# Performance work log

Measured on AMD Instinct MI355X. Metric: run time of the kernel, lower is better.

The kernel has to match this reference:

```python
import jax, jax.numpy as jnp
import numpy as np

WS = 7
NUM_HEADS = 12
DIM = 384
HEAD_DIM = DIM // NUM_HEADS
SCALE = HEAD_DIM ** -0.5


def _rel_pos_index(ws: int) -> jnp.ndarray:
    coords = np.stack(np.meshgrid(np.arange(ws), np.arange(ws), indexing='ij'))  # (2, ws, ws)
    cf = coords.reshape(2, -1)                       # (2, ws*ws)
    rel = cf[:, :, None] - cf[:, None, :]            # (2, N, N)
    rel = rel.transpose(1, 2, 0).copy()              # (N, N, 2)
    rel[..., 0] += ws - 1
    rel[..., 1] += ws - 1
    rel[..., 0] *= 2 * ws - 1
    return jnp.asarray(rel.sum(-1))                  # (N, N) int indices into bias table


REL_IDX = _rel_pos_index(WS)


def setup_inputs() -> dict:
    key = jax.random.key(0)
    ks = jax.random.split(key, 7)
    BW, N, C = 4096, WS * WS, DIM
    num_win = 64
    return {
        'x': jax.random.normal(ks[0], (BW, N, C), jnp.float32),
        'mask': jax.random.normal(ks[1], (num_win, N, N), jnp.float32),
        'qkv_w': jax.random.normal(ks[2], (3 * C, C), jnp.float32) * 0.02,
        'qkv_b': jax.random.normal(ks[3], (3 * C,), jnp.float32) * 0.02,
        'proj_w': jax.random.normal(ks[4], (C, C), jnp.float32) * 0.02,
        'proj_b': jax.random.normal(ks[5], (C,), jnp.float32) * 0.02,
        'bias_table': jax.random.normal(ks[6], ((2 * WS - 1) ** 2, NUM_HEADS), jnp.float32) * 0.02,
    }


def reference(x, mask, qkv_w, qkv_b, proj_w, proj_b, bias_table):
    BW, N, C = x.shape
    H, hd = NUM_HEADS, HEAD_DIM
    # QKV projection: (BW, N, 3C) -> (3, BW, H, N, hd)
    qkv = (x @ qkv_w.T + qkv_b).reshape(BW, N, 3, H, hd).transpose(2, 0, 3, 1, 4)
    q, k, v = qkv[0], qkv[1], qkv[2]
    attn = jnp.einsum('bhnd,bhmd->bhnm', q, k) * SCALE  # (BW, H, N, N)
    bias = bias_table[REL_IDX]                          # (N, N, H)
    attn = attn + bias.transpose(2, 0, 1)[None]
    num_win = mask.shape[0]
    attn = attn.reshape(BW // num_win, num_win, H, N, N) + mask[None, :, None]
    attn = attn.reshape(BW, H, N, N)
    attn = jax.nn.softmax(attn, axis=-1)
    out = jnp.einsum('bhnm,bhmd->bhnd', attn, v)        # (BW, H, N, hd)
    out = out.transpose(0, 2, 1, 3).reshape(BW, N, C)
    return out @ proj_w.T + proj_b
```

## Files before the change

### kernel.cpp

```cpp
#include <hip/hip_runtime.h>

typedef unsigned short u16;
typedef unsigned int u32;
typedef __attribute__((ext_vector_type(8))) short short8;
typedef __attribute__((ext_vector_type(4))) float floatx4;
typedef __attribute__((ext_vector_type(4))) unsigned int u32x4;

#define SCALE_Q 0.17677669529663687f

__device__ __forceinline__ u16 f2bf(float f) {
  u32 u = __float_as_uint(f);
  u = (u + 0x7fffu + ((u >> 16) & 1u)) >> 16;
  return (u16)u;
}

__device__ __forceinline__ void gload_lds16(const void* g, void* l) {
  __builtin_amdgcn_global_load_lds(
      (const __attribute__((address_space(1))) u32*)g,
      (__attribute__((address_space(3))) u32*)l, 16, 0, 0);
}

__device__ __forceinline__ floatx4 mfma16(short8 a, short8 b, floatx4 c) {
  return __builtin_amdgcn_mfma_f32_16x16x32_bf16(a, b, c, 0, 0, 0);
}

__global__ void cast_w_kernel(const float* __restrict__ qkv_w,
                              const float* __restrict__ proj_w,
                              u16* __restrict__ wb1, u16* __restrict__ wb2) {
  int idx = blockIdx.x * 256 + threadIdx.x;
  wb1[idx] = f2bf(qkv_w[idx]);
  if (idx < 147456) wb2[idx] = f2bf(proj_w[idx]);
}

__global__ __launch_bounds__(256) void cast_x_kernel(const float* __restrict__ x,
                                                     u16* __restrict__ xb) {
  const size_t i = ((size_t)blockIdx.x * 256 + threadIdx.x) * 8;
  const float4 f0 = *(const float4*)(x + i);
  const float4 f1 = *(const float4*)(x + i + 4);
  uint4 pk;
  pk.x = (u32)f2bf(f0.x) | ((u32)f2bf(f0.y) << 16);
  pk.y = (u32)f2bf(f0.z) | ((u32)f2bf(f0.w) << 16);
  pk.z = (u32)f2bf(f1.x) | ((u32)f2bf(f1.y) << 16);
  pk.w = (u32)f2bf(f1.z) | ((u32)f2bf(f1.w) << 16);
  *(uint4*)(xb + i) = pk;
}

__global__ void comb_kernel(const float* __restrict__ bias_table,
                            const float* __restrict__ mask,
                            float* __restrict__ comb) {
  int wh = blockIdx.x;
  int w = wh / 12, h = wh - w * 12;
  float* dst = comb + (size_t)wh * 4096;
  for (int e = threadIdx.x; e < 4096; e += 256) {
    int p = e >> 6, q = e & 63;
    float v;
    if (q >= 49) v = -1e30f;
    else if (p >= 49) v = 0.0f;
    else {
      int pi = p / 7, pj = p - pi * 7;
      int qi = q / 7, qj = q - qi * 7;
      int ridx = (pi - qi + 6) * 13 + (pj - qj + 6);
      v = bias_table[ridx * 12 + h] + mask[(size_t)w * 2401 + p * 49 + q];
    }
    dst[e] = v;
  }
}

__global__ __launch_bounds__(256) void qkv_gemm(const u16* __restrict__ A,
                                                const u16* __restrict__ B,
                                                const float* __restrict__ bias,
                                                u16* __restrict__ C) {
  __shared__ u16 As[2][4096];
  __shared__ u16 Bs[2][4096];
  const int tid = threadIdx.x;
  const int lane = tid & 63;
  const int wave = tid >> 6;
  const int l15 = lane & 15;
  const int quad = lane >> 4;
  const int wr = wave >> 1, wc = wave & 1;
  const u32 bid = blockIdx.x;
  const u32 xcd = bid & 7;
  const u32 slot = bid >> 3;
  const u32 grp = slot / 9;
  const u32 tn = slot - grp * 9;
  const u32 tm = xcd * 196 + grp;

  const int c0 = tid, c1 = tid + 256;
  const int m0 = c0 >> 2, kp0 = (c0 & 3) ^ ((m0 >> 1) & 3);
  const int m1 = c1 >> 2, kp1 = (c1 & 3) ^ ((m1 >> 1) & 3);
  const u16* Ab0 = A + (size_t)(tm * 128 + m0) * 384 + kp0 * 8;
  const u16* Ab1 = A + (size_t)(tm * 128 + m1) * 384 + kp1 * 8;
  const u16* Bb0 = B + (size_t)(tn * 128 + m0) * 384 + kp0 * 8;
  const u16* Bb1 = B + (size_t)(tn * 128 + m1) * 384 + kp1 * 8;
  const int ld0 = c0 * 8, ld1 = c1 * 8;

  floatx4 acc[4][4];
#pragma unroll
  for (int i = 0; i < 4; ++i)
#pragma unroll
    for (int j = 0; j < 4; ++j) acc[i][j] = (floatx4){0.f, 0.f, 0.f, 0.f};

#define QSTAGE(buf, k0)                       \
  do {                                        \
    gload_lds16(Ab0 + (k0), &As[buf][ld0]);   \
    gload_lds16(Ab1 + (k0), &As[buf][ld1]);   \
    gload_lds16(Bb0 + (k0), &Bs[buf][ld0]);   \
    gload_lds16(Bb1 + (k0), &Bs[buf][ld1]);   \
  } while (0)

  QSTAGE(0, 0);
  __syncthreads();

  const int xq = quad ^ ((l15 >> 1) & 3);
  const int abase = (wr * 64 + l15) * 32 + xq * 8;
  const int bbase = (wc * 64 + l15) * 32 + xq * 8;
  for (int kb = 0; kb < 12; ++kb) {
    const int cur = kb & 1;
    if (kb < 11) QSTAGE(cur ^ 1, (kb + 1) * 32);
    short8 af[4], bfr[4];
#pragma unroll
    for (int i = 0; i < 4; ++i)
      af[i] = *(const short8*)(&As[cur][abase + i * 512]);
#pragma unroll
    for (int i = 0; i < 4; ++i)
      bfr[i] = *(const short8*)(&Bs[cur][bbase + i * 512]);
#pragma unroll
    for (int mi = 0; mi < 4; ++mi)
#pragma unroll
      for (int ni = 0; ni < 4; ++ni)
        acc[mi][ni] = mfma16(af[mi], bfr[ni], acc[mi][ni]);
    if (kb < 11) __syncthreads();
  }
#undef QSTAGE

#pragma unroll
  for (int ni = 0; ni < 4; ++ni) {
    const int gbase = (int)tn * 128 + wc * 64 + ni * 16;
    const int which = gbase / 384;
    const int rem = gbase - which * 384;
    const int h = rem >> 5;
    const int db = rem & 31;
    const float bb = bias[gbase + l15];
    const float scale = (which == 0) ? SCALE_Q : 1.0f;
    u16* hp = C + ((size_t)which * 49152 + h) * 1568 + db + l15;
#pragma unroll
    for (int mi = 0; mi < 4; ++mi) {
      const int grow0 = (int)tm * 128 + wr * 64 + mi * 16 + quad * 4;
#pragma unroll
      for (int r = 0; r < 4; ++r) {
        const int grow = grow0 + r;
        const int b = grow / 49;
        const int tok = grow - b * 49;
        hp[(size_t)b * 18816 + tok * 32] = f2bf((acc[mi][ni][r] + bb) * scale);
      }
    }
  }
}

__global__ __launch_bounds__(256, 2) void attn_proj(const u16* __restrict__ qkv,
                                                    const float* __restrict__ comb,
                                                    const u16* __restrict__ pw,
                                                    const float* __restrict__ pb,
                                                    float* __restrict__ out) {
  __shared__ uint4 smem[4288];
  u16* aoS = (u16*)smem;
  const int tid = threadIdx.x;
  const int lane = tid & 63;
  const int wv = tid >> 6;
  const int l15 = lane & 15, quad = lane >> 4;
  u16* Vt = (u16*)((char*)smem + 50176 + wv * 4608);

  const int bid = blockIdx.x;
  const int w = bid >> 6;
  const int b = (bid & 63) * 64 + w;

  {
    uint4* v4 = (uint4*)Vt;
    const uint4 zz = make_uint4(0u, 0u, 0u, 0u);
    for (int i = lane; i < 288; i += 64) v4[i] = zz;
  }

  const floatx4 z4 = (floatx4){0.f, 0.f, 0.f, 0.f};
  const short8 z8 = {0, 0, 0, 0, 0, 0, 0, 0};

  for (int hi = 0; hi < 3; ++hi) {
    const int h = wv + hi * 4;
    const size_t hoff = (size_t)(b * 12 + h) * 1568;
    const u16* qb = qkv + hoff;
    const u16* kbp = qkv + (size_t)49152 * 1568 + hoff;
    const u16* vb = qkv + (size_t)98304 * 1568 + hoff;

    short8 aq[4], bk[4];
#pragma unroll
    for (int i = 0; i < 3; ++i) {
      aq[i] = *(const short8*)(qb + (i * 16 + l15) * 32 + quad * 8);
      bk[i] = *(const short8*)(kbp + (i * 16 + l15) * 32 + quad * 8);
    }
    aq[3] = (l15 == 0) ? *(const short8*)(qb + 48 * 32 + quad * 8) : z8;
    bk[3] = (l15 == 0) ? *(const short8*)(kbp + 48 * 32 + quad * 8) : z8;

    for (int s0 = lane; s0 < 196; s0 += 64) {
      const int t = s0 >> 2, part = s0 & 3;
      const uint4 dv = *(const uint4*)(vb + t * 32 + part * 8);
      const int d0 = part * 8;
      const u32 vv[4] = {dv.x, dv.y, dv.z, dv.w};
#pragma unroll
      for (int e = 0; e < 4; ++e) {
        Vt[(d0 + 2 * e) * 72 + t] = (u16)(vv[e] & 0xffffu);
        Vt[(d0 + 2 * e + 1) * 72 + t] = (u16)(vv[e] >> 16);
      }
    }

    floatx4 st[4][4];
    __builtin_amdgcn_s_setprio(1);
#pragma unroll
    for (int mi = 0; mi < 4; ++mi)
#pragma unroll
      for (int ni = 0; ni < 4; ++ni) st[mi][ni] = mfma16(bk[mi], aq[ni], z4);
    __builtin_amdgcn_s_setprio(0);

    const float* cb = comb + (size_t)(w * 12 + h) * 4096;
#pragma unroll
    for (int ni = 0; ni < 4; ++ni)
#pragma unroll
      for (int mi = 0; mi < 4; ++mi) {
        const float4 cv = *(const float4*)(cb + (ni * 16 + l15) * 64 + mi * 16 + quad * 4);
        st[mi][ni][0] += cv.x;
        st[mi][ni][1] += cv.y;
        st[mi][ni][2] += cv.z;
        st[mi][ni][3] += cv.w;
      }

    float rinv[4];
#pragma unroll
    for (int ni = 0; ni < 4; ++ni) {
      float mx = st[0][ni][0];
#pragma unroll
      for (int mi = 0; mi < 4; ++mi)
#pragma unroll
        for (int r = 0; r < 4; ++r) mx = fmaxf(mx, st[mi][ni][r]);
      mx = fmaxf(mx, __shfl_xor(mx, 16));
      mx = fmaxf(mx, __shfl_xor(mx, 32));
      float sum = 0.f;
#pragma unroll
      for (int mi = 0; mi < 4; ++mi)
#pragma unroll
        for (int r = 0; r < 4; ++r) {
          const float e = __expf(st[mi][ni][r] - mx);
          st[mi][ni][r] = e;
          sum += e;
        }
      sum += __shfl_xor(sum, 16);
      sum += __shfl_xor(sum, 32);
      rinv[ni] = 1.0f / sum;
    }

    u32 pk[4][4][2];
#pragma unroll
    for (int mi = 0; mi < 4; ++mi)
#pragma unroll
      for (int ni = 0; ni < 4; ++ni)
#pragma unroll
        for (int t = 0; t < 2; ++t)
          pk[mi][ni][t] = (u32)f2bf(st[mi][ni][2 * t] * rinv[ni]) |
                          ((u32)f2bf(st[mi][ni][2 * t + 1] * rinv[ni]) << 16);

    floatx4 ot[2][4];
#pragma unroll
    for (int mb = 0; mb < 2; ++mb)
#pragma unroll
      for (int nb = 0; nb < 4; ++nb) ot[mb][nb] = z4;

    const int srcLo = ((quad & 1) * 2) * 16 + l15;
    const int srcHi = srcLo + 16;
    const bool hiSel = (quad >> 1) != 0;
#pragma unroll
    for (int kk = 0; kk < 2; ++kk) {
      short8 av[2];
#pragma unroll
      for (int mb = 0; mb < 2; ++mb)
        av[mb] = *(const short8*)(Vt + (mb * 16 + l15) * 72 + kk * 32 + quad * 8);
#pragma unroll
      for (int nb = 0; nb < 4; ++nb) {
        const int ma = kk * 2, mbx = kk * 2 + 1;
        const u32 a0 = __shfl(pk[ma][nb][0], srcLo), b0 = __shfl(pk[mbx][nb][0], srcLo);
        const u32 a1 = __shfl(pk[ma][nb][1], srcLo), b1 = __shfl(pk[mbx][nb][1], srcLo);
        const u32 a2 = __shfl(pk[ma][nb][0], srcHi), b2 = __shfl(pk[mbx][nb][0], srcHi);
        const u32 a3 = __shfl(pk[ma][nb][1], srcHi), b3 = __shfl(pk[mbx][nb][1], srcHi);
        u32x4 tv = {hiSel ? b0 : a0, hiSel ? b1 : a1, hiSel ? b2 : a2, hiSel ? b3 : a3};
        const short8 pbv = __builtin_bit_cast(short8, tv);
        __builtin_amdgcn_s_setprio(1);
#pragma unroll
        for (int mb = 0; mb < 2; ++mb) ot[mb][nb] = mfma16(av[mb], pbv, ot[mb][nb]);
        __builtin_amdgcn_s_setprio(0);
      }
    }

#pragma unroll
    for (int mb = 0; mb < 2; ++mb)
#pragma unroll
      for (int nb = 0; nb < 4; ++nb) {
        const u32 lo = (u32)f2bf(ot[mb][nb][0]) | ((u32)f2bf(ot[mb][nb][1]) << 16);
        const u32 hi2 = (u32)f2bf(ot[mb][nb][2]) | ((u32)f2bf(ot[mb][nb][3]) << 16);
        uint2 uv;
        uv.x = lo;
        uv.y = hi2;
        *(uint2*)(aoS + (nb * 16 + l15) * 392 + h * 32 + mb * 16 + quad * 4) = uv;
      }
  }

  __syncthreads();

  floatx4 pacc[4][6];
#pragma unroll
  for (int mi = 0; mi < 4; ++mi)
#pragma unroll
    for (int nf = 0; nf < 6; ++nf) pacc[mi][nf] = z4;

  const u16* pwb = pw + (size_t)(wv * 96 + l15) * 384 + quad * 8;
#pragma unroll
  for (int kb = 0; kb < 12; ++kb) {
    short8 paf[4], pbf[6];
#pragma unroll
    for (int mi = 0; mi < 4; ++mi)
      paf[mi] = *(const short8*)(aoS + (mi * 16 + l15) * 392 + kb * 32 + quad * 8);
#pragma unroll
    for (int nf = 0; nf < 6; ++nf)
      pbf[nf] = *(const short8*)(pwb + nf * 6144 + kb * 32);
    __builtin_amdgcn_s_setprio(1);
#pragma unroll
    for (int mi = 0; mi < 4; ++mi)
#pragma unroll
      for (int nf = 0; nf < 6; ++nf)
        pacc[mi][nf] = mfma16(paf[mi], pbf[nf], pacc[mi][nf]);
    __builtin_amdgcn_s_setprio(0);
  }

#pragma unroll
  for (int nf = 0; nf < 6; ++nf) {
    const int col = wv * 96 + nf * 16 + l15;
    const float bb = pb[col];
#pragma unroll
    for (int mi = 0; mi < 4; ++mi)
#pragma unroll
      for (int r = 0; r < 4; ++r) {
        const int row = mi * 16 + quad * 4 + r;
        if (row < 49)
          out[((size_t)b * 49 + row) * 384 + col] = pacc[mi][nf][r] + bb;
      }
  }
}

extern "C" void kernel_launch(void* const* d_in, const int* in_sizes, int n_in,
                              void* d_out, int out_size, void* d_ws, size_t ws_size,
                              hipStream_t stream) {
  const float* x = (const float*)d_in[0];
  const float* mask = (const float*)d_in[1];
  const float* qkv_w = (const float*)d_in[2];
  const float* qkv_b = (const float*)d_in[3];
  const float* proj_w = (const float*)d_in[4];
  const float* proj_b = (const float*)d_in[5];
  const float* bias_table = (const float*)d_in[6];
  float* out = (float*)d_out;
  char* ws = (char*)d_ws;

  u16* wb1 = (u16*)(ws);
  u16* wb2 = (u16*)(ws + 884736);
  float* comb = (float*)(ws + 1179648);
  u16* qkvb = (u16*)(ws + 13762560);
  u16* xb = (u16*)(ws + 476184576);

  hipLaunchKernelGGL(cast_w_kernel, dim3(1728), dim3(256), 0, stream, qkv_w, proj_w, wb1, wb2);
  hipLaunchKernelGGL(cast_x_kernel, dim3(37632), dim3(256), 0, stream, x, xb);
  hipLaunchKernelGGL(comb_kernel, dim3(768), dim3(256), 0, stream, bias_table, mask, comb);
  hipLaunchKernelGGL(qkv_gemm, dim3(14112), dim3(256), 0, stream, xb, wb1, qkv_b, qkvb);
  hipLaunchKernelGGL(attn_proj, dim3(4096), dim3(256), 0, stream, qkvb, comb, wb2, proj_b, out);
}
```

Before: 1.194 ms.

## Fuse x bf16 cast into QKV GEMM and prefetch per-head QKV in attention

Removes the separate cast_x kernel. The QKV GEMM now loads fp32 x directly into registers, converts it to bf16 and writes it into LDS, with the next k-slice prefetched into registers. The GEMM loses its LDS double buffer and gains an extra barrier per k-step. The attention kernel also prefetches the next head's Q/K/V into registers, replacing the strided V loop and the Vt zero-init. This raises register pressure, and the GEMM now reads x in fp32 rather than bf16 on each of the 9 N-tiles that share a row block.

```diff
diff --git a/kernel.cpp b/kernel.cpp
--- a/kernel.cpp
+++ b/kernel.cpp
@@ -12,6 +12,10 @@
   u32 u = __float_as_uint(f);
   u = (u + 0x7fffu + ((u >> 16) & 1u)) >> 16;
   return (u16)u;
+}
+
+__device__ __forceinline__ u32 pk2bf(float lo, float hi) {
+  return (u32)f2bf(lo) | ((u32)f2bf(hi) << 16);
 }
 
 __device__ __forceinline__ void gload_lds16(const void* g, void* l) {
@@ -30,19 +34,6 @@
   int idx = blockIdx.x * 256 + threadIdx.x;
   wb1[idx] = f2bf(qkv_w[idx]);
   if (idx < 147456) wb2[idx] = f2bf(proj_w[idx]);
-}
-
-__global__ __launch_bounds__(256) void cast_x_kernel(const float* __restrict__ x,
-                                                     u16* __restrict__ xb) {
-  const size_t i = ((size_t)blockIdx.x * 256 + threadIdx.x) * 8;
-  const float4 f0 = *(const float4*)(x + i);
-  const float4 f1 = *(const float4*)(x + i + 4);
-  uint4 pk;
-  pk.x = (u32)f2bf(f0.x) | ((u32)f2bf(f0.y) << 16);
-  pk.y = (u32)f2bf(f0.z) | ((u32)f2bf(f0.w) << 16);
-  pk.z = (u32)f2bf(f1.x) | ((u32)f2bf(f1.y) << 16);
-  pk.w = (u32)f2bf(f1.z) | ((u32)f2bf(f1.w) << 16);
-  *(uint4*)(xb + i) = pk;
 }
 
 __global__ void comb_kernel(const float* __restrict__ bias_table,
@@ -66,12 +57,12 @@
   }
 }
 
-__global__ __launch_bounds__(256) void qkv_gemm(const u16* __restrict__ A,
+__global__ __launch_bounds__(256) void qkv_gemm(const float* __restrict__ X,
                                                 const u16* __restrict__ B,
                                                 const float* __restrict__ bias,
                                                 u16* __restrict__ C) {
-  __shared__ u16 As[2][4096];
-  __shared__ u16 Bs[2][4096];
+  __shared__ u16 As[4096];
+  __shared__ u16 Bs[4096];
   const int tid = threadIdx.x;
   const int lane = tid & 63;
   const int wave = tid >> 6;
@@ -85,11 +76,15 @@
   const u32 tn = slot - grp * 9;
   const u32 tm = xcd * 196 + grp;
 
+  const int mA = tid >> 1, hA = tid & 1;
+  const float* Axp = X + (size_t)(tm * 128 + mA) * 384 + hA * 16;
+  const int mskA = (mA >> 1) & 3;
+  const int sA0 = (mA * 4 + ((hA * 2) ^ mskA)) * 8;
+  const int sA1 = (mA * 4 + ((hA * 2 + 1) ^ mskA)) * 8;
+
   const int c0 = tid, c1 = tid + 256;
   const int m0 = c0 >> 2, kp0 = (c0 & 3) ^ ((m0 >> 1) & 3);
   const int m1 = c1 >> 2, kp1 = (c1 & 3) ^ ((m1 >> 1) & 3);
-  const u16* Ab0 = A + (size_t)(tm * 128 + m0) * 384 + kp0 * 8;
-  const u16* Ab1 = A + (size_t)(tm * 128 + m1) * 384 + kp1 * 8;
   const u16* Bb0 = B + (size_t)(tn * 128 + m0) * 384 + kp0 * 8;
   const u16* Bb1 = B + (size_t)(tn * 128 + m1) * 384 + kp1 * 8;
   const int ld0 = c0 * 8, ld1 = c1 * 8;
@@ -100,38 +95,52 @@
 #pragma unroll
     for (int j = 0; j < 4; ++j) acc[i][j] = (floatx4){0.f, 0.f, 0.f, 0.f};
 
-#define QSTAGE(buf, k0)                       \
-  do {                                        \
-    gload_lds16(Ab0 + (k0), &As[buf][ld0]);   \
-    gload_lds16(Ab1 + (k0), &As[buf][ld1]);   \
-    gload_lds16(Bb0 + (k0), &Bs[buf][ld0]);   \
-    gload_lds16(Bb1 + (k0), &Bs[buf][ld1]);   \
-  } while (0)
-
-  QSTAGE(0, 0);
-  __syncthreads();
+  float4 ar0 = *(const float4*)(Axp + 0);
+  float4 ar1 = *(const float4*)(Axp + 4);
+  float4 ar2 = *(const float4*)(Axp + 8);
+  float4 ar3 = *(const float4*)(Axp + 12);
 
   const int xq = quad ^ ((l15 >> 1) & 3);
   const int abase = (wr * 64 + l15) * 32 + xq * 8;
   const int bbase = (wc * 64 + l15) * 32 + xq * 8;
+
   for (int kb = 0; kb < 12; ++kb) {
-    const int cur = kb & 1;
-    if (kb < 11) QSTAGE(cur ^ 1, (kb + 1) * 32);
+    if (kb) __syncthreads();
+    const int k0 = kb * 32;
+    gload_lds16(Bb0 + k0, &Bs[ld0]);
+    gload_lds16(Bb1 + k0, &Bs[ld1]);
+    uint4 pA0, pA1;
+    pA0.x = pk2bf(ar0.x, ar0.y);
+    pA0.y = pk2bf(ar0.z, ar0.w);
+    pA0.z = pk2bf(ar1.x, ar1.y);
+    pA0.w = pk2bf(ar1.z, ar1.w);
+    pA1.x = pk2bf(ar2.x, ar2.y);
+    pA1.y = pk2bf(ar2.z, ar2.w);
+    pA1.z = pk2bf(ar3.x, ar3.y);
+    pA1.w = pk2bf(ar3.z, ar3.w);
+    *(uint4*)(&As[sA0]) = pA0;
+    *(uint4*)(&As[sA1]) = pA1;
+    if (kb < 11) {
+      const float* nx = Axp + (kb + 1) * 32;
+      ar0 = *(const float4*)(nx + 0);
+      ar1 = *(const float4*)(nx + 4);
+      ar2 = *(const float4*)(nx + 8);
+      ar3 = *(const float4*)(nx + 12);
+    }
+    __syncthreads();
     short8 af[4], bfr[4];
 #pragma unroll
     for (int i = 0; i < 4; ++i)
-      af[i] = *(const short8*)(&As[cur][abase + i * 512]);
+      af[i] = *(const short8*)(&As[abase + i * 512]);
 #pragma unroll
     for (int i = 0; i < 4; ++i)
-      bfr[i] = *(const short8*)(&Bs[cur][bbase + i * 512]);
+      bfr[i] = *(const short8*)(&Bs[bbase + i * 512]);
 #pragma unroll
     for (int mi = 0; mi < 4; ++mi)
 #pragma unroll
       for (int ni = 0; ni < 4; ++ni)
         acc[mi][ni] = mfma16(af[mi], bfr[ni], acc[mi][ni]);
-    if (kb < 11) __syncthreads();
-  }
-#undef QSTAGE
+  }
 
 #pragma unroll
   for (int ni = 0; ni < 4; ++ni) {
@@ -174,40 +183,57 @@
   const int w = bid >> 6;
   const int b = (bid & 63) * 64 + w;
 
-  {
-    uint4* v4 = (uint4*)Vt;
-    const uint4 zz = make_uint4(0u, 0u, 0u, 0u);
-    for (int i = lane; i < 288; i += 64) v4[i] = zz;
-  }
-
   const floatx4 z4 = (floatx4){0.f, 0.f, 0.f, 0.f};
   const short8 z8 = {0, 0, 0, 0, 0, 0, 0, 0};
 
+  const int vcol = (lane & 3) * 8;
+  const int vrow = lane >> 2;
+  const int voff0 = vrow * 32 + vcol;
+
+  short8 aqR[2][4], bkR[2][4];
+  uint4 vvR[2][4];
+
+#define LOADH(HH, RR)                                                          \
+  do {                                                                         \
+    const int h_ = wv + (HH) * 4;                                              \
+    const size_t ho_ = (size_t)(b * 12 + h_) * 1568;                           \
+    const u16* qb_ = qkv + ho_;                                                \
+    const u16* kb_ = qkv + (size_t)49152 * 1568 + ho_;                         \
+    const u16* vb_ = qkv + (size_t)98304 * 1568 + ho_;                         \
+    _Pragma("unroll") for (int i_ = 0; i_ < 3; ++i_) {                         \
+      aqR[RR][i_] = *(const short8*)(qb_ + (i_ * 16 + l15) * 32 + quad * 8);   \
+      bkR[RR][i_] = *(const short8*)(kb_ + (i_ * 16 + l15) * 32 + quad * 8);   \
+    }                                                                          \
+    aqR[RR][3] = (l15 == 0) ? *(const short8*)(qb_ + 48 * 32 + quad * 8) : z8; \
+    bkR[RR][3] = (l15 == 0) ? *(const short8*)(kb_ + 48 * 32 + quad * 8) : z8; \
+    vvR[RR][0] = *(const uint4*)(vb_ + voff0);                                 \
+    vvR[RR][1] = *(const uint4*)(vb_ + voff0 + 16 * 32);                       \
+    vvR[RR][2] = *(const uint4*)(vb_ + voff0 + 32 * 32);                       \
+    vvR[RR][3] = *(const uint4*)(vb_ + 48 * 32 + vcol);                        \
+  } while (0)
+
+  LOADH(0, 0);
+
+#pragma unroll
   for (int hi = 0; hi < 3; ++hi) {
+    const int cu = hi & 1;
     const int h = wv + hi * 4;
-    const size_t hoff = (size_t)(b * 12 + h) * 1568;
-    const u16* qb = qkv + hoff;
-    const u16* kbp = qkv + (size_t)49152 * 1568 + hoff;
-    const u16* vb = qkv + (size_t)98304 * 1568 + hoff;
-
-    short8 aq[4], bk[4];
-#pragma unroll
-    for (int i = 0; i < 3; ++i) {
-      aq[i] = *(const short8*)(qb + (i * 16 + l15) * 32 + quad * 8);
-      bk[i] = *(const short8*)(kbp + (i * 16 + l15) * 32 + quad * 8);
-    }
-    aq[3] = (l15 == 0) ? *(const short8*)(qb + 48 * 32 + quad * 8) : z8;
-    bk[3] = (l15 == 0) ? *(const short8*)(kbp + 48 * 32 + quad * 8) : z8;
-
-    for (int s0 = lane; s0 < 196; s0 += 64) {
-      const int t = s0 >> 2, part = s0 & 3;
-      const uint4 dv = *(const uint4*)(vb + t * 32 + part * 8);
-      const int d0 = part * 8;
-      const u32 vv[4] = {dv.x, dv.y, dv.z, dv.w};
+    if (hi < 2) {
+      if (hi == 0) LOADH(1, 1);
+      else LOADH(2, 0);
+    }
+
+#pragma unroll
+    for (int svi = 0; svi < 4; ++svi) {
+      uint4 dv = vvR[cu][svi];
+      const int t = vrow + svi * 16;
+      if (svi == 3 && lane >= 4) dv = make_uint4(0u, 0u, 0u, 0u);
+      const int d0 = (lane & 3) * 8;
+      const u32 vvx[4] = {dv.x, dv.y, dv.z, dv.w};
 #pragma unroll
       for (int e = 0; e < 4; ++e) {
-        Vt[(d0 + 2 * e) * 72 + t] = (u16)(vv[e] & 0xffffu);
-        Vt[(d0 + 2 * e + 1) * 72 + t] = (u16)(vv[e] >> 16);
+        Vt[(d0 + 2 * e) * 72 + t] = (u16)(vvx[e] & 0xffffu);
+        Vt[(d0 + 2 * e + 1) * 72 + t] = (u16)(vvx[e] >> 16);
       }
     }
 
@@ -216,7 +242,7 @@
 #pragma unroll
     for (int mi = 0; mi < 4; ++mi)
 #pragma unroll
-      for (int ni = 0; ni < 4; ++ni) st[mi][ni] = mfma16(bk[mi], aq[ni], z4);
+      for (int ni = 0; ni < 4; ++ni) st[mi][ni] = mfma16(bkR[cu][mi], aqR[cu][ni], z4);
     __builtin_amdgcn_s_setprio(0);
 
     const float* cb = comb + (size_t)(w * 12 + h) * 4096;
@@ -262,8 +288,8 @@
       for (int ni = 0; ni < 4; ++ni)
 #pragma unroll
         for (int t = 0; t < 2; ++t)
-          pk[mi][ni][t] = (u32)f2bf(st[mi][ni][2 * t] * rinv[ni]) |
-                          ((u32)f2bf(st[mi][ni][2 * t + 1] * rinv[ni]) << 16);
+          pk[mi][ni][t] = pk2bf(st[mi][ni][2 * t] * rinv[ni],
+                                st[mi][ni][2 * t + 1] * rinv[ni]);
 
     floatx4 ot[2][4];
 #pragma unroll
@@ -300,14 +326,13 @@
     for (int mb = 0; mb < 2; ++mb)
 #pragma unroll
       for (int nb = 0; nb < 4; ++nb) {
-        const u32 lo = (u32)f2bf(ot[mb][nb][0]) | ((u32)f2bf(ot[mb][nb][1]) << 16);
-        const u32 hi2 = (u32)f2bf(ot[mb][nb][2]) | ((u32)f2bf(ot[mb][nb][3]) << 16);
         uint2 uv;
-        uv.x = lo;
-        uv.y = hi2;
+        uv.x = pk2bf(ot[mb][nb][0], ot[mb][nb][1]);
+        uv.y = pk2bf(ot[mb][nb][2], ot[mb][nb][3]);
         *(uint2*)(aoS + (nb * 16 + l15) * 392 + h * 32 + mb * 16 + quad * 4) = uv;
       }
   }
+#undef LOADH
 
   __syncthreads();
 
@@ -368,11 +393,9 @@
   u16* wb2 = (u16*)(ws + 884736);
   float* comb = (float*)(ws + 1179648);
   u16* qkvb = (u16*)(ws + 13762560);
-  u16* xb = (u16*)(ws + 476184576);
 
   hipLaunchKernelGGL(cast_w_kernel, dim3(1728), dim3(256), 0, stream, qkv_w, proj_w, wb1, wb2);
-  hipLaunchKernelGGL(cast_x_kernel, dim3(37632), dim3(256), 0, stream, x, xb);
   hipLaunchKernelGGL(comb_kernel, dim3(768), dim3(256), 0, stream, bias_table, mask, comb);
-  hipLaunchKernelGGL(qkv_gemm, dim3(14112), dim3(256), 0, stream, xb, wb1, qkv_b, qkvb);
+  hipLaunchKernelGGL(qkv_gemm, dim3(14112), dim3(256), 0, stream, x, wb1, qkv_b, qkvb);
   hipLaunchKernelGGL(attn_proj, dim3(4096), dim3(256), 0, stream, qkvb, comb, wb2, proj_b, out);
 }
```

New measurement: 1.148 ms. -3.8%, faster.
